# Performance work log

Hardware: AMD Instinct MI355X
Metric: run time of the kernel (lower is better)

Reference implementation:

```python
import jax, jax.numpy as jnp
import numpy as np

GAMMA = 20.0
NUM_VIEWS = 64

def setup_inputs() -> dict:
    key = jax.random.key(0)
    k1, k2, k3 = jax.random.split(key, 3)
    B, L, D = 16, 4096, 1024
    v_pad = jax.random.normal(k1, (B, L, D), dtype=jnp.float32)
    v_len = jax.random.randint(k2, (B,), 1, L + 1, dtype=jnp.int32)
    # (T, H, W) per sample; only W/H ratio matters -> square 64x64 grid
    grid_thws = jnp.tile(jnp.array([[1, 64, 64]], dtype=jnp.int32), (B, 1))
    centers = jax.random.uniform(k3, (B, NUM_VIEWS, 2), dtype=jnp.float32)
    return {"v_pad": v_pad, "v_len": v_len, "grid_thws": grid_thws, "centers": centers}

def reference(v_pad, v_len, grid_thws, centers):
    B, L, D = v_pad.shape
    Lv = v_len.astype(jnp.float32)                      # [B]
    H = grid_thws[:, 1].astype(jnp.float32)
    W = grid_thws[:, 2].astype(jnp.float32)
    # adaptive 2D mapping of the 1D token sequence
    W_eff = jnp.maximum(1, jnp.round(jnp.sqrt(Lv * (W / H))).astype(jnp.int32))  # [B]
    H_eff = jnp.maximum(1, jnp.ceil(Lv / W_eff.astype(jnp.float32)).astype(jnp.int32))
    idx = jnp.arange(L, dtype=jnp.int32)                # [L]
    We = W_eff[:, None]
    He = H_eff[:, None]
    x = (idx[None, :] % We).astype(jnp.float32) / We.astype(jnp.float32)   # [B, L]
    y = (idx[None, :] // We).astype(jnp.float32) / He.astype(jnp.float32)  # [B, L]
    coords = jnp.stack([x, y], axis=-1)                 # [B, L, 2]
    # squared distance from each view center to each token coord
    diff = centers[:, :, None, :] - coords[:, None, :, :]   # [B, V, L, 2]
    dist_sq = jnp.sum(diff * diff, axis=-1)                 # [B, V, L]
    valid = (idx[None, :] < v_len[:, None]).astype(v_pad.dtype)  # [B, L]
    m = jnp.exp(-GAMMA * dist_sq) * valid[:, None, :]       # [B, V, L]
    numerator = jnp.einsum('bvl,bld->bvd', m, v_pad)        # [B, V, D]
    denominator = jnp.sum(m, axis=-1, keepdims=True) + 1e-6 # [B, V, 1]
    return numerator / denominator
```

## Files before the change

### kernel.cpp

```cpp
#include <hip/hip_runtime.h>
#include <hip/hip_bf16.h>
#include <math.h>
#include <stdint.h>


constexpr int VV  = 64;
constexpr int DC  = 128;
constexpr int KS  = 64;
constexpr int NTH = 256;
constexpr int ST2 = 134;
constexpr int KCH = 8;

typedef __attribute__((ext_vector_type(8))) short short8;
typedef __attribute__((ext_vector_type(4))) float f32x4;

static __device__ __forceinline__ unsigned short f2bf(float f) {
    __hip_bfloat16 h = __float2bfloat16(f);
    return __builtin_bit_cast(unsigned short, h);
}

__global__ __launch_bounds__(256)
void dvs_prep(const int* __restrict__ v_len, const int* __restrict__ gthw,
              const float* __restrict__ centers,
              unsigned short* __restrict__ mws,
              float* __restrict__ den_tile,
              int NT)
{
    const int t = blockIdx.x, b = blockIdx.y;
    const int Lv = v_len[b];
    const int lt = t * KS;
    if (lt >= Lv) return;

    const float Hf = (float)gthw[b*3 + 1];
    const float Wf = (float)gthw[b*3 + 2];
    const float sq = sqrtf((float)Lv * (Wf / Hf));
    int W_eff = (int)rintf(sq);                       if (W_eff < 1) W_eff = 1;
    int H_eff = (int)ceilf((float)Lv / (float)W_eff); if (H_eff < 1) H_eff = 1;
    const float invW = 1.f / (float)W_eff, invH = 1.f / (float)H_eff;

    const int tid  = threadIdx.x;
    const int lane = tid & 63, wave = tid >> 6;
    const int ar = lane & 15, koct = lane >> 4;

    __shared__ float sden[2][4][VV];

    short8* mtile = (short8*)mws + ((size_t)b * NT + t) * 8 * 64;

#pragma unroll
    for (int i = 0; i < 2; ++i) {
        const int f  = wave * 2 + i;
        const int ks = f >> 2, mf = f & 3;
        const int v  = mf * 16 + ar;
        const float2 ctr = ((const float2*)centers)[(size_t)b * VV + v];

        int l   = lt + ks * 32 + koct * 8;
        int row = l / W_eff;
        int col = l - row * W_eff;
        float y = (float)row * invH;

        union { unsigned short h[8]; short8 s; } ap;
        float ds = 0.f;
#pragma unroll
        for (int j = 0; j < 8; ++j) {
            float m = 0.f;
            if (l + j < Lv) {
                const float x  = (float)col * invW;
                const float dx = ctr.x - x, dy = ctr.y - y;
                m = __expf(-20.f * (dx * dx + dy * dy));
            }
            ds += m;
            ap.h[j] = f2bf(m);
            if (++col == W_eff) { col = 0; ++row; y = (float)row * invH; }
        }
        mtile[f * 64 + lane] = ap.s;
        sden[ks][koct][v] = ds;
    }
    __syncthreads();
    if (tid < VV) {
        float s = 0.f;
#pragma unroll
        for (int ks = 0; ks < 2; ++ks)
#pragma unroll
            for (int q = 0; q < 4; ++q) s += sden[ks][q][tid];
        den_tile[((size_t)b * NT + t) * VV + tid] = s;
    }
}

__global__ __launch_bounds__(NTH)
void dvs_mfma(const float* __restrict__ v_pad, const int* __restrict__ v_len,
              const unsigned short* __restrict__ mws,
              const float* __restrict__ den_tile,
              float* __restrict__ num_part,
              float* __restrict__ den_part,
              int L, int D, int NT)
{
    const int kblk = blockIdx.x, dcb = blockIdx.y, b = blockIdx.z;
    const int Lv = v_len[b];
    const int chunk = (((Lv + KCH - 1) / KCH) + 63) & ~63;
    const int l0 = kblk * chunk;
    if (l0 >= Lv) return;
    const int l1 = min(l0 + chunk, Lv);

    const int tid  = threadIdx.x;
    const int d0   = dcb * DC;
    const int lane = tid & 63;
    const int wave = tid >> 6;

    __shared__ __align__(16) unsigned short smB[KS][ST2];

    const int sd   = tid & 31;
    const int srow = tid >> 5;
    const int fcol = lane & 15, foct = lane >> 4;

    f32x4 acc[4][2];
#pragma unroll
    for (int i = 0; i < 4; ++i) {
        acc[i][0] = f32x4{0.f, 0.f, 0.f, 0.f};
        acc[i][1] = f32x4{0.f, 0.f, 0.f, 0.f};
    }
    float denacc = 0.f;

    const float*  vp_b   = v_pad + (size_t)b * L * D + d0;
    const short8* mws_b  = (const short8*)mws + (size_t)b * NT * 8 * 64;
    const float*  dt_b   = den_tile + (size_t)b * NT * VV;

    float4 ld[8];
#pragma unroll
    for (int it = 0; it < 8; ++it) {
        const int l = l0 + it * 8 + srow;
        ld[it] = make_float4(0.f, 0.f, 0.f, 0.f);
        if (l < l1)
            ld[it] = *(const float4*)(vp_b + (size_t)l * D + sd * 4);
    }

    for (int lt = l0; lt < l1; lt += KS) {
#pragma unroll
        for (int it = 0; it < 8; ++it) {
            const int lrow = it * 8 + srow;
            unsigned* w = (unsigned*)&smB[lrow][sd * 4];
            w[0] = (unsigned)f2bf(ld[it].x) | ((unsigned)f2bf(ld[it].y) << 16);
            w[1] = (unsigned)f2bf(ld[it].z) | ((unsigned)f2bf(ld[it].w) << 16);
        }
        __syncthreads();

        const int ltn = lt + KS;
        if (ltn < l1) {
#pragma unroll
            for (int it = 0; it < 8; ++it) {
                const int l = ltn + it * 8 + srow;
                ld[it] = make_float4(0.f, 0.f, 0.f, 0.f);
                if (l < l1)
                    ld[it] = *(const float4*)(vp_b + (size_t)l * D + sd * 4);
            }
        }

        const short8* mt = mws_b + ((size_t)(lt >> 6)) * 8 * 64;
        short8 af[2][4];
#pragma unroll
        for (int ks = 0; ks < 2; ++ks)
#pragma unroll
            for (int mf = 0; mf < 4; ++mf)
                af[ks][mf] = mt[(ks * 4 + mf) * 64 + lane];

        if (dcb == 0 && tid < VV)
            denacc += dt_b[(size_t)(lt >> 6) * VV + tid];

#pragma unroll
        for (int ks = 0; ks < 2; ++ks) {
#pragma unroll
            for (int nf = 0; nf < 2; ++nf) {
                const int colx  = wave * 32 + nf * 16 + fcol;
                const int kbase = ks * 32 + foct * 8;
                union { unsigned short h[8]; short8 s; } bf;
#pragma unroll
                for (int j = 0; j < 8; ++j)
                    bf.h[j] = smB[kbase + j][colx];
#pragma unroll
                for (int mf = 0; mf < 4; ++mf)
                    acc[mf][nf] = __builtin_amdgcn_mfma_f32_16x16x32_bf16(
                        af[ks][mf], bf.s, acc[mf][nf], 0, 0, 0);
            }
        }
        __syncthreads();
    }

    if (dcb == 0 && tid < VV)
        den_part[((size_t)b * KCH + kblk) * VV + tid] = denacc;

    float* basep = num_part + ((size_t)b * KCH + kblk) * VV * (size_t)D + d0 + wave * 32;
#pragma unroll
    for (int mf = 0; mf < 4; ++mf) {
#pragma unroll
        for (int nf = 0; nf < 2; ++nf) {
            const int colx = nf * 16 + fcol;
            const int row0 = mf * 16 + foct * 4;
#pragma unroll
            for (int r = 0; r < 4; ++r)
                basep[(size_t)(row0 + r) * D + colx] = acc[mf][nf][r];
        }
    }
}

__global__ __launch_bounds__(256)
void dvs_reduce(const float* __restrict__ num_part,
                const float* __restrict__ den_part,
                const int*   __restrict__ v_len,
                float*       __restrict__ out,
                int D, int total4)
{
    const int idx = blockIdx.x * 256 + threadIdx.x;
    if (idx >= total4) return;
    const int dq4 = D / 4;
    const int d4  = idx % dq4;
    const int bv  = idx / dq4;
    const int b   = bv / VV;
    const int v   = bv - b * VV;

    const int Lv    = v_len[b];
    const int chunk = (((Lv + KCH - 1) / KCH) + 63) & ~63;
    const int nk    = (Lv + chunk - 1) / chunk;

    float  den = 1e-6f;
    float4 num = make_float4(0.f, 0.f, 0.f, 0.f);
    for (int k = 0; k < nk; ++k) {
        den += den_part[((size_t)b * KCH + k) * VV + v];
        const float4 p = ((const float4*)(num_part +
                          (((size_t)b * KCH + k) * VV + v) * (size_t)D))[d4];
        num.x += p.x; num.y += p.y; num.z += p.z; num.w += p.w;
    }
    const float inv = 1.0f / den;
    ((float4*)out)[(size_t)bv * dq4 + d4] =
        make_float4(num.x * inv, num.y * inv, num.z * inv, num.w * inv);
}

extern "C" void kernel_launch(void* const* d_in, const int* in_sizes, int n_in,
                              void* d_out, int out_size, void* d_ws, size_t ws_size,
                              hipStream_t stream)
{
    const float* v_pad     = (const float*)d_in[0];
    const int*   v_len     = (const int*)d_in[1];
    const int*   grid_thws = (const int*)d_in[2];
    const float* centers   = (const float*)d_in[3];
    float*       out       = (float*)d_out;

    const int B  = in_sizes[1];
    const int D  = out_size / (B * VV);
    const int L  = in_sizes[0] / (B * D);
    const int NT = (L + KS - 1) / KS;

    float*          num_part = (float*)d_ws;
    float*          den_part = num_part + (size_t)B * KCH * VV * D;
    float*          den_tile = den_part + (size_t)B * KCH * VV;
    unsigned short* mws      = (unsigned short*)(den_tile + (size_t)B * NT * VV);

    dim3 gridP(NT, B);
    dvs_prep<<<gridP, 256, 0, stream>>>(v_len, grid_thws, centers, mws,
                                        den_tile, NT);

    dim3 gridG(KCH, D / DC, B);
    dvs_mfma<<<gridG, NTH, 0, stream>>>(v_pad, v_len, mws, den_tile,
                                        num_part, den_part, L, D, NT);

    const int total4 = B * VV * D / 4;
    dvs_reduce<<<(total4 + 255) / 256, 256, 0, stream>>>(num_part, den_part,
                                                         v_len, out, D, total4);
}
```

Measured before the change: 42.77 us.

## Store partial sums in fp16, move denominator sum into reduce, flatten grid order

```diff
diff --git a/kernel.cpp b/kernel.cpp
--- a/kernel.cpp
+++ b/kernel.cpp
@@ -13,6 +13,8 @@
 
 typedef __attribute__((ext_vector_type(8))) short short8;
 typedef __attribute__((ext_vector_type(4))) float f32x4;
+typedef _Float16 f16;
+typedef __attribute__((ext_vector_type(4))) _Float16 f16x4;
 
 static __device__ __forceinline__ unsigned short f2bf(float f) {
     __hip_bfloat16 h = __float2bfloat16(f);
@@ -89,12 +91,15 @@
 __global__ __launch_bounds__(NTH)
 void dvs_mfma(const float* __restrict__ v_pad, const int* __restrict__ v_len,
               const unsigned short* __restrict__ mws,
-              const float* __restrict__ den_tile,
-              float* __restrict__ num_part,
-              float* __restrict__ den_part,
+              f16* __restrict__ num_part,
               int L, int D, int NT)
 {
-    const int kblk = blockIdx.x, dcb = blockIdx.y, b = blockIdx.z;
+    const int flat = blockIdx.x;
+    const int kblk = flat >> 7;
+    const int g    = flat & 127;
+    const int dcb  = g & 7;
+    const int b    = g >> 3;
+
     const int Lv = v_len[b];
     const int chunk = (((Lv + KCH - 1) / KCH) + 63) & ~63;
     const int l0 = kblk * chunk;
@@ -118,11 +123,9 @@
         acc[i][0] = f32x4{0.f, 0.f, 0.f, 0.f};
         acc[i][1] = f32x4{0.f, 0.f, 0.f, 0.f};
     }
-    float denacc = 0.f;
-
-    const float*  vp_b   = v_pad + (size_t)b * L * D + d0;
-    const short8* mws_b  = (const short8*)mws + (size_t)b * NT * 8 * 64;
-    const float*  dt_b   = den_tile + (size_t)b * NT * VV;
+
+    const float*  vp_b  = v_pad + (size_t)b * L * D + d0;
+    const short8* mws_b = (const short8*)mws + (size_t)b * NT * 8 * 64;
 
     float4 ld[8];
 #pragma unroll
@@ -162,9 +165,6 @@
             for (int mf = 0; mf < 4; ++mf)
                 af[ks][mf] = mt[(ks * 4 + mf) * 64 + lane];
 
-        if (dcb == 0 && tid < VV)
-            denacc += dt_b[(size_t)(lt >> 6) * VV + tid];
-
 #pragma unroll
         for (int ks = 0; ks < 2; ++ks) {
 #pragma unroll
@@ -184,10 +184,7 @@
         __syncthreads();
     }
 
-    if (dcb == 0 && tid < VV)
-        den_part[((size_t)b * KCH + kblk) * VV + tid] = denacc;
-
-    float* basep = num_part + ((size_t)b * KCH + kblk) * VV * (size_t)D + d0 + wave * 32;
+    f16* basep = num_part + ((size_t)b * KCH + kblk) * VV * (size_t)D + d0 + wave * 32;
 #pragma unroll
     for (int mf = 0; mf < 4; ++mf) {
 #pragma unroll
@@ -196,40 +193,63 @@
             const int row0 = mf * 16 + foct * 4;
 #pragma unroll
             for (int r = 0; r < 4; ++r)
-                basep[(size_t)(row0 + r) * D + colx] = acc[mf][nf][r];
+                basep[(size_t)(row0 + r) * D + colx] = (f16)acc[mf][nf][r];
         }
     }
 }
 
 __global__ __launch_bounds__(256)
-void dvs_reduce(const float* __restrict__ num_part,
-                const float* __restrict__ den_part,
+void dvs_reduce(const f16* __restrict__ num_part,
+                const float* __restrict__ den_tile,
                 const int*   __restrict__ v_len,
                 float*       __restrict__ out,
-                int D, int total4)
-{
-    const int idx = blockIdx.x * 256 + threadIdx.x;
-    if (idx >= total4) return;
-    const int dq4 = D / 4;
-    const int d4  = idx % dq4;
-    const int bv  = idx / dq4;
-    const int b   = bv / VV;
-    const int v   = bv - b * VV;
+                int D, int NT)
+{
+    const int flat = blockIdx.x;
+    const int vg  = flat >> 7;
+    const int gg  = flat & 127;
+    const int dcb = gg & 7;
+    const int b   = gg >> 3;
+
+    const int tid = threadIdx.x;
+    const int vi  = tid >> 5;
+    const int c4  = tid & 31;
+    const int v   = vg * 8 + vi;
 
     const int Lv    = v_len[b];
     const int chunk = (((Lv + KCH - 1) / KCH) + 63) & ~63;
     const int nk    = (Lv + chunk - 1) / chunk;
-
-    float  den = 1e-6f;
+    const int nt    = (Lv + KS - 1) / KS;
+
+    __shared__ float sp[8][8];
+    __shared__ float sinv[8];
+    if (tid < 64) {
+        const int vd = vg * 8 + (tid & 7);
+        const int part = tid >> 3;
+        float s = 0.f;
+        for (int t = part; t < nt; t += 8)
+            s += den_tile[((size_t)b * NT + t) * VV + vd];
+        sp[tid & 7][part] = s;
+    }
+    __syncthreads();
+    if (tid < 8) {
+        float s = 1e-6f;
+#pragma unroll
+        for (int p = 0; p < 8; ++p) s += sp[tid][p];
+        sinv[tid] = 1.0f / s;
+    }
+    __syncthreads();
+
+    const int dof = dcb * DC + c4 * 4;
     float4 num = make_float4(0.f, 0.f, 0.f, 0.f);
     for (int k = 0; k < nk; ++k) {
-        den += den_part[((size_t)b * KCH + k) * VV + v];
-        const float4 p = ((const float4*)(num_part +
-                          (((size_t)b * KCH + k) * VV + v) * (size_t)D))[d4];
-        num.x += p.x; num.y += p.y; num.z += p.z; num.w += p.w;
-    }
-    const float inv = 1.0f / den;
-    ((float4*)out)[(size_t)bv * dq4 + d4] =
+        const f16x4 p = *(const f16x4*)(num_part +
+            (((size_t)b * KCH + k) * VV + v) * (size_t)D + dof);
+        num.x += (float)p[0]; num.y += (float)p[1];
+        num.z += (float)p[2]; num.w += (float)p[3];
+    }
+    const float inv = sinv[vi];
+    *(float4*)(out + ((size_t)b * VV + v) * (size_t)D + dof) =
         make_float4(num.x * inv, num.y * inv, num.z * inv, num.w * inv);
 }
 
@@ -248,20 +268,17 @@
     const int L  = in_sizes[0] / (B * D);
     const int NT = (L + KS - 1) / KS;
 
-    float*          num_part = (float*)d_ws;
-    float*          den_part = num_part + (size_t)B * KCH * VV * D;
-    float*          den_tile = den_part + (size_t)B * KCH * VV;
+    f16*            num_part = (f16*)d_ws;
+    float*          den_tile = (float*)(num_part + (size_t)B * KCH * VV * D);
     unsigned short* mws      = (unsigned short*)(den_tile + (size_t)B * NT * VV);
 
     dim3 gridP(NT, B);
     dvs_prep<<<gridP, 256, 0, stream>>>(v_len, grid_thws, centers, mws,
                                         den_tile, NT);
 
-    dim3 gridG(KCH, D / DC, B);
-    dvs_mfma<<<gridG, NTH, 0, stream>>>(v_pad, v_len, mws, den_tile,
-                                        num_part, den_part, L, D, NT);
-
-    const int total4 = B * VV * D / 4;
-    dvs_reduce<<<(total4 + 255) / 256, 256, 0, stream>>>(num_part, den_part,
-                                                         v_len, out, D, total4);
-}
+    const int nblkG = KCH * (D / DC) * B;
+    dvs_mfma<<<nblkG, NTH, 0, stream>>>(v_pad, v_len, mws, num_part, L, D, NT);
+
+    const int nblkR = 8 * (D / DC) * B;
+    dvs_reduce<<<nblkR, 256, 0, stream>>>(num_part, den_tile, v_len, out, D, NT);
+}
```

Result: slower. 48.27 us (+12.9%).

## Double-buffer v_pad prefetch two tiles ahead and move denominator sum to reduce

Applied to the files above, without the earlier changes.

```diff
diff --git a/kernel.cpp b/kernel.cpp
--- a/kernel.cpp
+++ b/kernel.cpp
@@ -89,9 +89,7 @@
 __global__ __launch_bounds__(NTH)
 void dvs_mfma(const float* __restrict__ v_pad, const int* __restrict__ v_len,
               const unsigned short* __restrict__ mws,
-              const float* __restrict__ den_tile,
               float* __restrict__ num_part,
-              float* __restrict__ den_part,
               int L, int D, int NT)
 {
     const int kblk = blockIdx.x, dcb = blockIdx.y, b = blockIdx.z;
@@ -118,41 +116,36 @@
         acc[i][0] = f32x4{0.f, 0.f, 0.f, 0.f};
         acc[i][1] = f32x4{0.f, 0.f, 0.f, 0.f};
     }
-    float denacc = 0.f;
-
-    const float*  vp_b   = v_pad + (size_t)b * L * D + d0;
-    const short8* mws_b  = (const short8*)mws + (size_t)b * NT * 8 * 64;
-    const float*  dt_b   = den_tile + (size_t)b * NT * VV;
-
-    float4 ld[8];
-#pragma unroll
-    for (int it = 0; it < 8; ++it) {
-        const int l = l0 + it * 8 + srow;
-        ld[it] = make_float4(0.f, 0.f, 0.f, 0.f);
-        if (l < l1)
-            ld[it] = *(const float4*)(vp_b + (size_t)l * D + sd * 4);
-    }
-
-    for (int lt = l0; lt < l1; lt += KS) {
+
+    const float*  vp_b  = v_pad + (size_t)b * L * D + d0;
+    const short8* mws_b = (const short8*)mws + (size_t)b * NT * 8 * 64;
+
+    float4 ld[2][8];
+
+#define ISSUE(SET, LT)                                                         \
+    _Pragma("unroll")                                                          \
+    for (int it = 0; it < 8; ++it) {                                           \
+        const int l = (LT) + it * 8 + srow;                                    \
+        ld[SET][it] = make_float4(0.f, 0.f, 0.f, 0.f);                         \
+        if (l < l1)                                                            \
+            ld[SET][it] = *(const float4*)(vp_b + (size_t)l * D + sd * 4);     \
+    }
+
+    ISSUE(0, l0);
+    if (l0 + KS < l1) { ISSUE(1, l0 + KS); }
+
+    int lt = l0, cur = 0;
+    for (; lt < l1; lt += KS, cur ^= 1) {
 #pragma unroll
         for (int it = 0; it < 8; ++it) {
             const int lrow = it * 8 + srow;
             unsigned* w = (unsigned*)&smB[lrow][sd * 4];
-            w[0] = (unsigned)f2bf(ld[it].x) | ((unsigned)f2bf(ld[it].y) << 16);
-            w[1] = (unsigned)f2bf(ld[it].z) | ((unsigned)f2bf(ld[it].w) << 16);
+            w[0] = (unsigned)f2bf(ld[cur][it].x) | ((unsigned)f2bf(ld[cur][it].y) << 16);
+            w[1] = (unsigned)f2bf(ld[cur][it].z) | ((unsigned)f2bf(ld[cur][it].w) << 16);
         }
         __syncthreads();
 
-        const int ltn = lt + KS;
-        if (ltn < l1) {
-#pragma unroll
-            for (int it = 0; it < 8; ++it) {
-                const int l = ltn + it * 8 + srow;
-                ld[it] = make_float4(0.f, 0.f, 0.f, 0.f);
-                if (l < l1)
-                    ld[it] = *(const float4*)(vp_b + (size_t)l * D + sd * 4);
-            }
-        }
+        if (lt + 2 * KS < l1) { ISSUE(cur, lt + 2 * KS); }
 
         const short8* mt = mws_b + ((size_t)(lt >> 6)) * 8 * 64;
         short8 af[2][4];
@@ -161,9 +154,6 @@
 #pragma unroll
             for (int mf = 0; mf < 4; ++mf)
                 af[ks][mf] = mt[(ks * 4 + mf) * 64 + lane];
-
-        if (dcb == 0 && tid < VV)
-            denacc += dt_b[(size_t)(lt >> 6) * VV + tid];
 
 #pragma unroll
         for (int ks = 0; ks < 2; ++ks) {
@@ -183,9 +173,7 @@
         }
         __syncthreads();
     }
-
-    if (dcb == 0 && tid < VV)
-        den_part[((size_t)b * KCH + kblk) * VV + tid] = denacc;
+#undef ISSUE
 
     float* basep = num_part + ((size_t)b * KCH + kblk) * VV * (size_t)D + d0 + wave * 32;
 #pragma unroll
@@ -203,33 +191,46 @@
 
 __global__ __launch_bounds__(256)
 void dvs_reduce(const float* __restrict__ num_part,
-                const float* __restrict__ den_part,
+                const float* __restrict__ den_tile,
                 const int*   __restrict__ v_len,
                 float*       __restrict__ out,
-                int D, int total4)
-{
-    const int idx = blockIdx.x * 256 + threadIdx.x;
-    if (idx >= total4) return;
-    const int dq4 = D / 4;
-    const int d4  = idx % dq4;
-    const int bv  = idx / dq4;
-    const int b   = bv / VV;
-    const int v   = bv - b * VV;
+                int D, int NT)
+{
+    const int bv = blockIdx.x;
+    const int b  = bv >> 6;
+    const int v  = bv & 63;
+    const int tid = threadIdx.x;
 
     const int Lv    = v_len[b];
     const int chunk = (((Lv + KCH - 1) / KCH) + 63) & ~63;
     const int nk    = (Lv + chunk - 1) / chunk;
-
-    float  den = 1e-6f;
+    const int nt    = (Lv + KS - 1) / KS;
+
+    __shared__ float s64[64];
+    __shared__ float sinv;
+    if (tid < 64) {
+        float s = 0.f;
+        for (int t = tid; t < nt; t += 64)
+            s += den_tile[((size_t)b * NT + t) * VV + v];
+        s64[tid] = s;
+    }
+    __syncthreads();
+    if (tid == 0) {
+        float s = 1e-6f;
+#pragma unroll
+        for (int i = 0; i < 64; ++i) s += s64[i];
+        sinv = 1.0f / s;
+    }
+    __syncthreads();
+
     float4 num = make_float4(0.f, 0.f, 0.f, 0.f);
+    const float* np = num_part + ((size_t)b * KCH * VV + v) * (size_t)D + tid * 4;
     for (int k = 0; k < nk; ++k) {
-        den += den_part[((size_t)b * KCH + k) * VV + v];
-        const float4 p = ((const float4*)(num_part +
-                          (((size_t)b * KCH + k) * VV + v) * (size_t)D))[d4];
+        const float4 p = *(const float4*)(np + (size_t)k * VV * D);
         num.x += p.x; num.y += p.y; num.z += p.z; num.w += p.w;
     }
-    const float inv = 1.0f / den;
-    ((float4*)out)[(size_t)bv * dq4 + d4] =
+    const float inv = sinv;
+    *(float4*)(out + (size_t)bv * D + tid * 4) =
         make_float4(num.x * inv, num.y * inv, num.z * inv, num.w * inv);
 }
 
@@ -249,8 +250,7 @@
     const int NT = (L + KS - 1) / KS;
 
     float*          num_part = (float*)d_ws;
-    float*          den_part = num_part + (size_t)B * KCH * VV * D;
-    float*          den_tile = den_part + (size_t)B * KCH * VV;
+    float*          den_tile = num_part + (size_t)B * KCH * VV * D;
     unsigned short* mws      = (unsigned short*)(den_tile + (size_t)B * NT * VV);
 
     dim3 gridP(NT, B);
@@ -258,10 +258,7 @@
                                         den_tile, NT);
 
     dim3 gridG(KCH, D / DC, B);
-    dvs_mfma<<<gridG, NTH, 0, stream>>>(v_pad, v_len, mws, den_tile,
-                                        num_part, den_part, L, D, NT);
-
-    const int total4 = B * VV * D / 4;
-    dvs_reduce<<<(total4 + 255) / 256, 256, 0, stream>>>(num_part, den_part,
-                                                         v_len, out, D, total4);
-}
+    dvs_mfma<<<gridG, NTH, 0, stream>>>(v_pad, v_len, mws, num_part, L, D, NT);
+
+    dvs_reduce<<<B * VV, 256, 0, stream>>>(num_part, den_tile, v_len, out, D, NT);
+}
```

Result: slower. 87.80 us (+105.3%).
